# Performance work log

Hardware: AMD Instinct MI355X
Metric: run time of the kernel (lower is better)

Reference implementation:

```python
import jax, jax.numpy as jnp
import numpy as np

NUM_ANCHORS = 3
NUM_CLASSES = 80


def setup_inputs() -> dict:
    key = jax.random.key(0)
    k1, _ = jax.random.split(key)
    B, C, G0, G1 = 16, NUM_ANCHORS * (NUM_CLASSES + 5), 64, 64
    x = jax.random.normal(k1, (B, C, G0, G1), dtype=jnp.float32)
    # normalized (w, h) anchor pairs, as in __init__
    anchors = jnp.array([[0.28, 0.22], [0.38, 0.48], [0.90, 0.78]], dtype=jnp.float32)
    return {"x": x, "anchors": anchors}


def reference(x, anchors):
    B = x.shape[0]
    A, nC = NUM_ANCHORS, NUM_CLASSES
    g0, g1 = x.shape[2], x.shape[3]
    # [B, A, g0, g1, 5+nC]
    pred = x.reshape(B, A, nC + 5, g0, g1).transpose(0, 1, 3, 4, 2)

    sx = jax.nn.sigmoid(pred[..., 0])
    sy = jax.nn.sigmoid(pred[..., 1])
    w = pred[..., 2]
    h = pred[..., 3]
    pred_conf = jax.nn.sigmoid(pred[..., 4])
    pred_cls = jax.nn.sigmoid(pred[..., 5:])

    # grid_x varies along axis 2 (row index), grid_y along axis 3 (col index),
    # matching the torch repeat/.t() construction in compute_grid_offsets.
    grid_x = jnp.arange(g0, dtype=x.dtype).reshape(1, 1, g0, 1)
    grid_y = jnp.arange(g1, dtype=x.dtype).reshape(1, 1, 1, g1)
    anchor_w = (anchors[:, 0] * g0).reshape(1, A, 1, 1)
    anchor_h = (anchors[:, 1] * g1).reshape(1, A, 1, 1)

    pred_boxes = jnp.stack(
        [
            sx + grid_x,
            sy + grid_y,
            jnp.exp(w) * anchor_w,
            jnp.exp(h) * anchor_h,
        ],
        axis=-1,
    )  # [B, A, g0, g1, 4]

    scale = jnp.array([g0, g1, g0, g1], dtype=x.dtype)
    return pred_boxes / scale, pred_conf, pred_cls
```

## Files before the change

### kernel.cpp

```cpp
#include <hip/hip_runtime.h>
#include <math.h>

#define NB 16
#define NA 3
#define NC 80
#define GS 4096
#define NPOS (NB * NA * GS)
#define LDS_S 65

__device__ __forceinline__ float sigmoidf_(float v) {
    return 1.0f / (1.0f + __expf(-v));
}

__global__ __launch_bounds__(256) void yolo_kernel(const float* __restrict__ x,
                                                   const float* __restrict__ anchors,
                                                   float* __restrict__ out) {
    __shared__ float lds[NC * LDS_S];
    const int tid  = threadIdx.x;
    const int ba   = blockIdx.x >> 6;
    const int tile = blockIdx.x & 63;
    const int s0   = tile << 6;
    const float* __restrict__ xb = x + (size_t)ba * 85 * GS + s0;

    #pragma unroll
    for (int k = 0; k < 5; ++k) {
        const int e4 = tid + k * 256;
        const int ch = e4 >> 4;
        const int p  = (e4 & 15) << 2;
        const float4 v = *reinterpret_cast<const float4*>(xb + (size_t)(5 + ch) * GS + p);
        float* l = lds + ch * LDS_S + p;
        l[0] = sigmoidf_(v.x);
        l[1] = sigmoidf_(v.y);
        l[2] = sigmoidf_(v.z);
        l[3] = sigmoidf_(v.w);
    }

    if (tid < 64) {
        const int p = tid;
        const int t = ba * GS + s0 + p;
        const float tx = xb[0 * GS + p];
        const float ty = xb[1 * GS + p];
        const float tw = xb[2 * GS + p];
        const float th = xb[3 * GS + p];
        const float tc = xb[4 * GS + p];
        const int a = ba % NA;
        const float aw = anchors[a * 2 + 0];
        const float ah = anchors[a * 2 + 1];
        float4 box;
        box.x = (sigmoidf_(tx) + (float)tile) * (1.0f / 64.0f);
        box.y = (sigmoidf_(ty) + (float)p)    * (1.0f / 64.0f);
        box.z = __expf(tw) * aw;
        box.w = __expf(th) * ah;
        reinterpret_cast<float4*>(out)[t] = box;
        out[NPOS * 4 + t] = sigmoidf_(tc);
    }

    __syncthreads();

    float4* __restrict__ out4 =
        reinterpret_cast<float4*>(out + (size_t)NPOS * 5 + (size_t)(ba * GS + s0) * NC);
    #pragma unroll
    for (int k = 0; k < 5; ++k) {
        const int o4 = tid + k * 256;
        const int o  = o4 * 4;
        const int p  = o / 80;
        const int ch = o - p * 80;
        float4 v;
        v.x = lds[(ch + 0) * LDS_S + p];
        v.y = lds[(ch + 1) * LDS_S + p];
        v.z = lds[(ch + 2) * LDS_S + p];
        v.w = lds[(ch + 3) * LDS_S + p];
        out4[o4] = v;
    }
}

extern "C" void kernel_launch(void* const* d_in, const int* in_sizes, int n_in,
                              void* d_out, int out_size, void* d_ws, size_t ws_size,
                              hipStream_t stream) {
    const float* x       = (const float*)d_in[0];
    const float* anchors = (const float*)d_in[1];
    float* out           = (float*)d_out;
    const int blocks = NB * NA * 64;
    yolo_kernel<<<blocks, 256, 0, stream>>>(x, anchors, out);
}
```

Baseline: 113.8 us.

## Partition LDS transpose per wave to replace block barrier with wave barrier

Each 64-lane wave now owns 16 spatial positions and its own LDS slice (stride 17), so it loads, applies the sigmoid and transposes only its own data. The block-wide __syncthreads is replaced by an lgkmcnt wait plus a wave barrier, so waves no longer stall on one another. Each wave's global loads shrink to 64-byte row segments per channel, which may hurt coalescing. LDS use grows slightly with the padding.

```diff
diff --git a/kernel.cpp b/kernel.cpp
--- a/kernel.cpp
+++ b/kernel.cpp
@@ -6,7 +6,8 @@
 #define NC 80
 #define GS 4096
 #define NPOS (NB * NA * GS)
-#define LDS_S 65
+#define CH_S 17
+#define WAVE_LDS (NC * CH_S)
 
 __device__ __forceinline__ float sigmoidf_(float v) {
     return 1.0f / (1.0f + __expf(-v));
@@ -15,28 +16,32 @@
 __global__ __launch_bounds__(256) void yolo_kernel(const float* __restrict__ x,
                                                    const float* __restrict__ anchors,
                                                    float* __restrict__ out) {
-    __shared__ float lds[NC * LDS_S];
+    __shared__ float lds[4 * WAVE_LDS];
     const int tid  = threadIdx.x;
+    const int lane = tid & 63;
+    const int w    = tid >> 6;
     const int ba   = blockIdx.x >> 6;
     const int tile = blockIdx.x & 63;
     const int s0   = tile << 6;
     const float* __restrict__ xb = x + (size_t)ba * 85 * GS + s0;
+    float* __restrict__ lw = lds + w * WAVE_LDS;
+    const int pw = w << 4;
 
     #pragma unroll
     for (int k = 0; k < 5; ++k) {
-        const int e4 = tid + k * 256;
-        const int ch = e4 >> 4;
-        const int p  = (e4 & 15) << 2;
-        const float4 v = *reinterpret_cast<const float4*>(xb + (size_t)(5 + ch) * GS + p);
-        float* l = lds + ch * LDS_S + p;
+        const int e4 = lane + (k << 6);
+        const int ch = e4 >> 2;
+        const int g  = (e4 & 3) << 2;
+        const float4 v = *reinterpret_cast<const float4*>(xb + (size_t)(5 + ch) * GS + pw + g);
+        float* l = lw + ch * CH_S + g;
         l[0] = sigmoidf_(v.x);
         l[1] = sigmoidf_(v.y);
         l[2] = sigmoidf_(v.z);
         l[3] = sigmoidf_(v.w);
     }
 
-    if (tid < 64) {
-        const int p = tid;
+    if (lane < 16) {
+        const int p = pw + lane;
         const int t = ba * GS + s0 + p;
         const float tx = xb[0 * GS + p];
         const float ty = xb[1 * GS + p];
@@ -55,21 +60,22 @@
         out[NPOS * 4 + t] = sigmoidf_(tc);
     }
 
-    __syncthreads();
+    asm volatile("s_waitcnt lgkmcnt(0)" ::: "memory");
+    __builtin_amdgcn_wave_barrier();
 
     float4* __restrict__ out4 =
-        reinterpret_cast<float4*>(out + (size_t)NPOS * 5 + (size_t)(ba * GS + s0) * NC);
+        reinterpret_cast<float4*>(out + (size_t)NPOS * 5 + (size_t)(ba * GS + s0 + pw) * NC);
     #pragma unroll
     for (int k = 0; k < 5; ++k) {
-        const int o4 = tid + k * 256;
+        const int o4 = lane + (k << 6);
         const int o  = o4 * 4;
         const int p  = o / 80;
         const int ch = o - p * 80;
         float4 v;
-        v.x = lds[(ch + 0) * LDS_S + p];
-        v.y = lds[(ch + 1) * LDS_S + p];
-        v.z = lds[(ch + 2) * LDS_S + p];
-        v.w = lds[(ch + 3) * LDS_S + p];
+        v.x = lw[(ch + 0) * CH_S + p];
+        v.y = lw[(ch + 1) * CH_S + p];
+        v.z = lw[(ch + 2) * CH_S + p];
+        v.w = lw[(ch + 3) * CH_S + p];
         out4[o4] = v;
     }
 }
```

Result: no change. 115.0 us (+1.1%).
